# Optimization experiments

Measured on AMD Instinct MI355X. Metric: run time of the kernel, lower is better.

The kernel has to match this reference:

```python
import jax, jax.numpy as jnp
import numpy as np

N_NODES = 10000
N_EDGES = 320000
HID = 256
EDGE_D = 2
NORM_FACTOR = 100.0
NORM_CONST = 1.0


def setup_inputs() -> dict:
    key = jax.random.key(0)
    ks = jax.random.split(key, 32)
    s = 0.02
    d = {
        'h': jax.random.normal(ks[0], (N_NODES, HID), jnp.float32),
        'x': jax.random.normal(ks[1], (N_NODES, 3), jnp.float32),
        'edge_index': jax.random.randint(ks[2], (2, N_EDGES), 0, N_NODES, jnp.int32),
        'edge_attr': jax.random.uniform(ks[3], (N_EDGES, EDGE_D), jnp.float32),
    }
    in_e = 2 * HID + EDGE_D  # 514
    ki = 4
    for li in range(2):
        p = f'gcl{li}_'
        d[p + 'ew1'] = jax.random.normal(ks[ki], (in_e, HID), jnp.float32) * s; ki += 1
        d[p + 'eb1'] = jnp.zeros((HID,), jnp.float32)
        d[p + 'ew2'] = jax.random.normal(ks[ki], (HID, HID), jnp.float32) * s; ki += 1
        d[p + 'eb2'] = jnp.zeros((HID,), jnp.float32)
        d[p + 'nw1'] = jax.random.normal(ks[ki], (2 * HID, HID), jnp.float32) * s; ki += 1
        d[p + 'nb1'] = jnp.zeros((HID,), jnp.float32)
        d[p + 'nw2'] = jax.random.normal(ks[ki], (HID, HID), jnp.float32) * s; ki += 1
        d[p + 'nb2'] = jnp.zeros((HID,), jnp.float32)
        d[p + 'aw'] = jax.random.normal(ks[ki], (HID, 1), jnp.float32) * s; ki += 1
        d[p + 'ab'] = jnp.zeros((1,), jnp.float32)
    d['cw1'] = jax.random.normal(ks[ki], (in_e, HID), jnp.float32) * s; ki += 1
    d['cb1'] = jnp.zeros((HID,), jnp.float32)
    d['cw2'] = jax.random.normal(ks[ki], (HID, HID), jnp.float32) * s; ki += 1
    d['cb2'] = jnp.zeros((HID,), jnp.float32)
    # xavier_uniform with gain=0.001 -> very small final layer
    d['cw3'] = jax.random.normal(ks[ki], (HID, 1), jnp.float32) * 0.001
    return d


def _gcl(h, row, col, edge_attr, ew1, eb1, ew2, eb2, nw1, nb1, nw2, nb2, aw, ab, n_nodes):
    inp = jnp.concatenate([h[row], h[col], edge_attr], axis=1)  # [E, 2H+2]
    mij = jax.nn.silu(jax.nn.silu(inp @ ew1 + eb1) @ ew2 + eb2)  # [E, H]
    att = jax.nn.sigmoid(mij @ aw + ab)                          # [E, 1]
    ef = mij * att
    agg = jax.ops.segment_sum(ef, row, num_segments=n_nodes) / NORM_FACTOR
    nin = jnp.concatenate([h, agg], axis=1)                      # [N, 2H]
    return h + (jax.nn.silu(nin @ nw1 + nb1) @ nw2 + nb2)


def reference(h, x, edge_index, edge_attr,
              gcl0_ew1, gcl0_eb1, gcl0_ew2, gcl0_eb2, gcl0_nw1, gcl0_nb1, gcl0_nw2, gcl0_nb2, gcl0_aw, gcl0_ab,
              gcl1_ew1, gcl1_eb1, gcl1_ew2, gcl1_eb2, gcl1_nw1, gcl1_nb1, gcl1_nw2, gcl1_nb2, gcl1_aw, gcl1_ab,
              cw1, cb1, cw2, cb2, cw3):
    n_nodes = h.shape[0]
    row, col = edge_index[0], edge_index[1]
    # coord2diff (norm_constant = 1)
    diff = x[row] - x[col]                                  # [E, 3]
    radial = jnp.sum(diff * diff, axis=1, keepdims=True)    # [E, 1]
    norm = jnp.sqrt(radial + 1e-8)
    coord_diff = diff / (norm + NORM_CONST)
    # two GCL layers (reflection_equiv=True -> no cross product)
    h = _gcl(h, row, col, edge_attr, gcl0_ew1, gcl0_eb1, gcl0_ew2, gcl0_eb2,
             gcl0_nw1, gcl0_nb1, gcl0_nw2, gcl0_nb2, gcl0_aw, gcl0_ab, n_nodes)
    h = _gcl(h, row, col, edge_attr, gcl1_ew1, gcl1_eb1, gcl1_ew2, gcl1_eb2,
             gcl1_nw1, gcl1_nb1, gcl1_nw2, gcl1_nb2, gcl1_aw, gcl1_ab, n_nodes)
    # equivariant coordinate update (tanh=False)
    inp = jnp.concatenate([h[row], h[col], edge_attr], axis=1)
    phi = jax.nn.silu(jax.nn.silu(inp @ cw1 + cb1) @ cw2 + cb2) @ cw3  # [E, 1]
    trans = coord_diff * phi                                            # [E, 3]
    agg = jax.ops.segment_sum(trans, row, num_segments=n_nodes) / NORM_FACTOR
    x = x + agg
    return h, x
```

## Files before the change

### kernel.cpp

```cpp
#include <hip/hip_runtime.h>
#include <hip/hip_fp16.h>
#include <stdint.h>

#define NN   10000
#define NE   320000
#define HID  256
#define MB   64
#define NEB  (NE/MB)
#define VST  264

#define DG_PLAIN 0
#define DG_SPLIT 1
#define DG_2A    2

typedef __attribute__((ext_vector_type(8))) short short8;
typedef __attribute__((ext_vector_type(4))) float f32x4;

struct CvtPtrs { const float* p[15]; };

__device__ __forceinline__ float silu_f(float v){ return v / (1.f + __expf(-v)); }
__device__ __forceinline__ float sigm_f(float v){ return 1.f / (1.f + __expf(-v)); }
__device__ __forceinline__ __half2 silu2(__half2 x){
    __half2 e = h2exp2(__hmul2(x, __float2half2_rn(-1.442695041f)));
    __half2 d = __hadd2(e, __float2half2_rn(1.0f));
    return __hmul2(x, h2rcp(d));
}

__global__ __launch_bounds__(256) void k_count(const int* __restrict__ row, int* __restrict__ cnt){
    int e = blockIdx.x * 256 + threadIdx.x;
    if (e < NE) atomicAdd(&cnt[row[e]], 1);
}

__global__ __launch_bounds__(256) void k_scan(const int* __restrict__ cnt, int* __restrict__ rs, int* __restrict__ cur){
    __shared__ int sums[256];
    const int PER = 40;
    int t = threadIdx.x;
    int base = t * PER;
    int s = 0;
    for (int i = 0; i < PER; i++){
        int idx = base + i;
        s += (idx < NN) ? cnt[idx] : 0;
    }
    sums[t] = s;
    __syncthreads();
    for (int off = 1; off < 256; off <<= 1){
        int v = (t >= off) ? sums[t - off] : 0;
        __syncthreads();
        sums[t] += v;
        __syncthreads();
    }
    int run = (t == 0) ? 0 : sums[t - 1];
    for (int i = 0; i < PER; i++){
        int idx = base + i;
        if (idx < NN){
            int c = cnt[idx];
            rs[idx] = run;
            cur[idx] = run;
            run += c;
        }
    }
    if (t == 255) rs[NN] = sums[255];
}

__global__ __launch_bounds__(256) void k_fill(const int* __restrict__ row, int* __restrict__ cur, int* __restrict__ perm){
    int e = blockIdx.x * 256 + threadIdx.x;
    if (e < NE){
        int p = atomicAdd(&cur[row[e]], 1);
        perm[p] = e;
    }
}

__global__ __launch_bounds__(256) void k_cvtw(CvtPtrs pp, __half* __restrict__ dst){
    int i = blockIdx.x * 256 + threadIdx.x;
    const float* src = pp.p[i >> 16];
    int t = i & 65535;
    int j = t & 7, lane = (t >> 3) & 63, kk = (t >> 9) & 7, nt = t >> 12;
    int k = kk * 32 + (lane >> 4) * 8 + j;
    int n = nt * 16 + (lane & 15);
    dst[i] = __float2half_rn(src[k * HID + n]);
}

__global__ __launch_bounds__(256) void k_cvt16(const float* __restrict__ src, __half* __restrict__ dst){
    int i = (blockIdx.x * 256 + threadIdx.x) * 8;
    float4 f0 = *(const float4*)&src[i];
    float4 f1 = *(const float4*)&src[i + 4];
    uint4 o; __half2* op = (__half2*)&o;
    op[0] = __float22half2_rn(make_float2(f0.x, f0.y));
    op[1] = __float22half2_rn(make_float2(f0.z, f0.w));
    op[2] = __float22half2_rn(make_float2(f1.x, f1.y));
    op[3] = __float22half2_rn(make_float2(f1.z, f1.w));
    *(uint4*)&dst[i] = o;
}

__global__ __launch_bounds__(256, 4) void k_dgemm(
        const __half* __restrict__ A1, const float* __restrict__ A2f,
        const __half* __restrict__ wpool, int wAidx, int wBidx,
        const float* __restrict__ bias, const float* __restrict__ R,
        float* __restrict__ out32, __half* __restrict__ out16,
        __half* __restrict__ outB16, int mode, int act){
    __shared__ __half alds[64 * VST];
    int tid = threadIdx.x;
    int lid = tid & 63, w = tid >> 6;
    int quad = lid >> 4, l15 = lid & 15;
    int rb = blockIdx.x * 64;
    int by = blockIdx.y;

    float bv[2]; int cg0[2];
    #pragma unroll
    for (int n = 0; n < 2; n++){
        int cg = by * 128 + w * 32 + n * 16 + l15;
        cg0[n] = cg;
        bv[n] = (bias && cg < 256) ? bias[cg] : 0.f;
    }
    f32x4 acc[4][2];
    #pragma unroll
    for (int m = 0; m < 4; m++)
        #pragma unroll
        for (int n = 0; n < 2; n++){ f32x4 z = {bv[n], bv[n], bv[n], bv[n]}; acc[m][n] = z; }

    int npass = (mode == DG_2A) ? 2 : 1;
    int sr = tid >> 5, c0 = (tid & 31) * 8;
    for (int pass = 0; pass < npass; pass++){
        if (pass) __syncthreads();
        int widx, byl = by;
        if (mode == DG_SPLIT){ if (by >= 2){ widx = wBidx; byl = by - 2; } else widx = wAidx; }
        else widx = pass ? wBidx : wAidx;
        const short8* bbase = (const short8*)(wpool + (size_t)widx * 65536);

        if (pass == 0){
            #pragma unroll
            for (int it = 0; it < 8; it++){
                int r = it * 8 + sr;
                int rr = rb + r; if (rr > NN - 1) rr = NN - 1;
                *(uint4*)&alds[r * VST + c0] = *(const uint4*)&A1[(size_t)rr * HID + c0];
            }
        } else {
            #pragma unroll
            for (int it = 0; it < 8; it++){
                int r = it * 8 + sr;
                int rr = rb + r; if (rr > NN - 1) rr = NN - 1;
                float4 f0 = *(const float4*)&A2f[(size_t)rr * HID + c0];
                float4 f1 = *(const float4*)&A2f[(size_t)rr * HID + c0 + 4];
                uint4 o; __half2* op = (__half2*)&o;
                op[0] = __float22half2_rn(make_float2(f0.x, f0.y));
                op[1] = __float22half2_rn(make_float2(f0.z, f0.w));
                op[2] = __float22half2_rn(make_float2(f1.x, f1.y));
                op[3] = __float22half2_rn(make_float2(f1.z, f1.w));
                *(uint4*)&alds[r * VST + c0] = o;
            }
        }
        __syncthreads();
        #pragma unroll
        for (int kk = 0; kk < 8; kk++){
            short8 bf[2];
            #pragma unroll
            for (int n = 0; n < 2; n++)
                bf[n] = bbase[((byl * 8 + w * 2 + n) * 8 + kk) * 64 + lid];
            #pragma unroll
            for (int m = 0; m < 4; m++){
                const short8 af = *(const short8*)&alds[(m * 16 + l15) * VST + kk * 32 + quad * 8];
                #pragma unroll
                for (int n = 0; n < 2; n++)
                    acc[m][n] = __builtin_amdgcn_mfma_f32_16x16x32_f16(af, bf[n], acc[m][n], 0, 0, 0);
            }
        }
    }
    #pragma unroll
    for (int n = 0; n < 2; n++){
        int cg = cg0[n];
        #pragma unroll
        for (int m = 0; m < 4; m++){
            #pragma unroll
            for (int r = 0; r < 4; r++){
                int rg = rb + m * 16 + quad * 4 + r;
                if (rg < NN){
                    float v = acc[m][n][r];
                    if (act) v = silu_f(v);
                    if (R) v += R[(size_t)rg * HID + cg];
                    if (mode == DG_SPLIT){
                        if (cg < 256) out16[(size_t)rg * HID + cg] = __float2half_rn(v);
                        else          outB16[(size_t)rg * HID + cg - 256] = __float2half_rn(v);
                    } else {
                        if (out32) out32[(size_t)rg * HID + cg] = v;
                        if (out16) out16[(size_t)rg * HID + cg] = __float2half_rn(v);
                    }
                }
            }
        }
    }
}

__global__ __launch_bounds__(256, 4) void k_edge_mfma(
        const __half* __restrict__ HrowB, const __half* __restrict__ HcolB,
        const int* __restrict__ row, const int* __restrict__ col,
        const float* __restrict__ ea, const int* __restrict__ perm,
        const __half* __restrict__ w2f,
        const float* __restrict__ w512, const float* __restrict__ w513,
        const float* __restrict__ eb2, const float* __restrict__ aw, const float* __restrict__ ab,
        float* __restrict__ agg){
    __shared__ __half vlds[MB * VST];
    __shared__ float attp[4][MB];
    __shared__ float attf[MB];
    __shared__ int   nrows[MB];
    __shared__ int   cids[MB];
    __shared__ float ea0s[MB], ea1s[MB];

    int tid = threadIdx.x;
    int e0  = blockIdx.x * MB;
    if (tid < MB){
        int eid = perm[e0 + tid];
        nrows[tid] = row[eid];
        cids[tid]  = col[eid];
        ea0s[tid]  = ea[eid * 2 + 0];
        ea1s[tid]  = ea[eid * 2 + 1];
    }
    __syncthreads();
    {
        int sr = tid >> 5;
        int c0 = (tid & 31) * 8;
        float4 wa = *(const float4*)&w512[c0];
        float4 wb = *(const float4*)&w512[c0 + 4];
        float4 ua = *(const float4*)&w513[c0];
        float4 ub = *(const float4*)&w513[c0 + 4];
        __half2 w5h[4] = {__float22half2_rn(make_float2(wa.x, wa.y)), __float22half2_rn(make_float2(wa.z, wa.w)),
                          __float22half2_rn(make_float2(wb.x, wb.y)), __float22half2_rn(make_float2(wb.z, wb.w))};
        __half2 w6h[4] = {__float22half2_rn(make_float2(ua.x, ua.y)), __float22half2_rn(make_float2(ua.z, ua.w)),
                          __float22half2_rn(make_float2(ub.x, ub.y)), __float22half2_rn(make_float2(ub.z, ub.w))};
        #pragma unroll
        for (int it = 0; it < 8; it++){
            int r = it * 8 + sr;
            int nid = nrows[r], cid = cids[r];
            __half2 e0h = __float2half2_rn(ea0s[r]);
            __half2 e1h = __float2half2_rn(ea1s[r]);
            uint4 hr4 = *(const uint4*)&HrowB[(size_t)nid * HID + c0];
            uint4 hc4 = *(const uint4*)&HcolB[(size_t)cid * HID + c0];
            const __half2* hrp = (const __half2*)&hr4;
            const __half2* hcp = (const __half2*)&hc4;
            uint4 o; __half2* op = (__half2*)&o;
            #pragma unroll
            for (int q = 0; q < 4; q++){
                __half2 t = __hadd2(hrp[q], hcp[q]);
                t = __hfma2(e0h, w5h[q], t);
                t = __hfma2(e1h, w6h[q], t);
                op[q] = silu2(t);
            }
            *(uint4*)&vlds[r * VST + c0] = o;
        }
    }
    __syncthreads();

    int lid = tid & 63, w = tid >> 6;
    int quad = lid >> 4, l15 = lid & 15;

    float b2v[4], awv[4];
    #pragma unroll
    for (int n = 0; n < 4; n++){
        int cg = w * 64 + n * 16 + l15;
        b2v[n] = eb2[cg]; awv[n] = aw[cg];
    }
    f32x4 acc[4][4];
    #pragma unroll
    for (int m = 0; m < 4; m++)
        #pragma unroll
        for (int n = 0; n < 4; n++){ f32x4 z = {b2v[n], b2v[n], b2v[n], b2v[n]}; acc[m][n] = z; }

    const short8* bbase = (const short8*)w2f;
    #pragma unroll
    for (int kk = 0; kk < 8; kk++){
        short8 bf[4];
        #pragma unroll
        for (int n = 0; n < 4; n++)
            bf[n] = bbase[((w * 4 + n) * 8 + kk) * 64 + lid];
        #pragma unroll
        for (int m = 0; m < 4; m++){
            const short8 af = *(const short8*)&vlds[(m * 16 + l15) * VST + kk * 32 + quad * 8];
            #pragma unroll
            for (int n = 0; n < 4; n++)
                acc[m][n] = __builtin_amdgcn_mfma_f32_16x16x32_f16(af, bf[n], acc[m][n], 0, 0, 0);
        }
    }

    #pragma unroll
    for (int m = 0; m < 4; m++){
        float p[4] = {0.f, 0.f, 0.f, 0.f};
        #pragma unroll
        for (int n = 0; n < 4; n++){
            #pragma unroll
            for (int r = 0; r < 4; r++){
                float mij = silu_f(acc[m][n][r]);
                acc[m][n][r] = mij;
                p[r] += mij * awv[n];
            }
        }
        #pragma unroll
        for (int r = 0; r < 4; r++){
            p[r] += __shfl_xor(p[r], 1);
            p[r] += __shfl_xor(p[r], 2);
            p[r] += __shfl_xor(p[r], 4);
            p[r] += __shfl_xor(p[r], 8);
        }
        if (l15 == 0){
            #pragma unroll
            for (int r = 0; r < 4; r++)
                attp[w][m * 16 + quad * 4 + r] = p[r];
        }
    }
    __syncthreads();
    if (tid < MB){
        float a0 = attp[0][tid] + attp[1][tid] + attp[2][tid] + attp[3][tid] + ab[0];
        attf[tid] = 0.01f * sigm_f(a0);
    }
    __syncthreads();

    for (int m = 0; m < 4; m++){
        int mb = m * 16;
        float av[4]; int nv[4];
        #pragma unroll
        for (int r = 0; r < 4; r++){
            av[r] = attf[mb + quad * 4 + r];
            nv[r] = nrows[mb + quad * 4 + r];
        }
        int rA = nrows[mb], rB = nrows[mb + 15];
        if (rA == rB){
            #pragma unroll
            for (int n = 0; n < 4; n++){
                float s = acc[m][n][0] * av[0] + acc[m][n][1] * av[1]
                        + acc[m][n][2] * av[2] + acc[m][n][3] * av[3];
                s += __shfl_xor(s, 16);
                s += __shfl_xor(s, 32);
                if (lid < 16)
                    atomicAdd(&agg[(size_t)rA * HID + w * 64 + n * 16 + lid], s);
            }
        } else {
            float ef[4][4];
            #pragma unroll
            for (int n = 0; n < 4; n++)
                #pragma unroll
                for (int r = 0; r < 4; r++)
                    ef[n][r] = acc[m][n][r] * av[r];
            int myn = nrows[mb + l15];
            int t16 = 0;
            while (t16 < 16){
                int tgt = nrows[mb + t16];
                unsigned long long bal = __ballot((lid < 16) && (lid > t16) && (myn != tgt));
                int nxt = bal ? (__ffsll((unsigned long long)bal) - 1) : 16;
                #pragma unroll
                for (int n = 0; n < 4; n++){
                    float s = 0.f;
                    #pragma unroll
                    for (int r = 0; r < 4; r++)
                        s += (nv[r] == tgt) ? ef[n][r] : 0.f;
                    s += __shfl_xor(s, 16);
                    s += __shfl_xor(s, 32);
                    if (lid < 16)
                        atomicAdd(&agg[(size_t)tgt * HID + w * 64 + n * 16 + lid], s);
                }
                t16 = nxt;
            }
        }
    }
}

__global__ __launch_bounds__(256, 4) void k_coord_mfma(
        const __half* __restrict__ CrowB, const __half* __restrict__ CcolB,
        const int* __restrict__ row, const int* __restrict__ col,
        const float* __restrict__ ea, const int* __restrict__ perm,
        const __half* __restrict__ w2f,
        const float* __restrict__ w512, const float* __restrict__ w513,
        const float* __restrict__ cb2, const float* __restrict__ cw3,
        float* __restrict__ phi){
    __shared__ __half vlds[MB * VST];
    __shared__ float pp[4][MB];
    __shared__ int   nrows[MB];
    __shared__ int   cids[MB];
    __shared__ float ea0s[MB], ea1s[MB];

    int tid = threadIdx.x;
    int e0  = blockIdx.x * MB;
    if (tid < MB){
        int eid = perm[e0 + tid];
        nrows[tid] = row[eid];
        cids[tid]  = col[eid];
        ea0s[tid]  = ea[eid * 2 + 0];
        ea1s[tid]  = ea[eid * 2 + 1];
    }
    __syncthreads();
    {
        int sr = tid >> 5;
        int c0 = (tid & 31) * 8;
        float4 wa = *(const float4*)&w512[c0];
        float4 wb = *(const float4*)&w512[c0 + 4];
        float4 ua = *(const float4*)&w513[c0];
        float4 ub = *(const float4*)&w513[c0 + 4];
        __half2 w5h[4] = {__float22half2_rn(make_float2(wa.x, wa.y)), __float22half2_rn(make_float2(wa.z, wa.w)),
                          __float22half2_rn(make_float2(wb.x, wb.y)), __float22half2_rn(make_float2(wb.z, wb.w))};
        __half2 w6h[4] = {__float22half2_rn(make_float2(ua.x, ua.y)), __float22half2_rn(make_float2(ua.z, ua.w)),
                          __float22half2_rn(make_float2(ub.x, ub.y)), __float22half2_rn(make_float2(ub.z, ub.w))};
        #pragma unroll
        for (int it = 0; it < 8; it++){
            int r = it * 8 + sr;
            int nid = nrows[r], cid = cids[r];
            __half2 e0h = __float2half2_rn(ea0s[r]);
            __half2 e1h = __float2half2_rn(ea1s[r]);
            uint4 hr4 = *(const uint4*)&CrowB[(size_t)nid * HID + c0];
            uint4 hc4 = *(const uint4*)&CcolB[(size_t)cid * HID + c0];
            const __half2* hrp = (const __half2*)&hr4;
            const __half2* hcp = (const __half2*)&hc4;
            uint4 o; __half2* op = (__half2*)&o;
            #pragma unroll
            for (int q = 0; q < 4; q++){
                __half2 t = __hadd2(hrp[q], hcp[q]);
                t = __hfma2(e0h, w5h[q], t);
                t = __hfma2(e1h, w6h[q], t);
                op[q] = silu2(t);
            }
            *(uint4*)&vlds[r * VST + c0] = o;
        }
    }
    __syncthreads();

    int lid = tid & 63, w = tid >> 6;
    int quad = lid >> 4, l15 = lid & 15;

    float b2v[4], w3v[4];
    #pragma unroll
    for (int n = 0; n < 4; n++){
        int cg = w * 64 + n * 16 + l15;
        b2v[n] = cb2[cg]; w3v[n] = cw3[cg];
    }
    f32x4 acc[4][4];
    #pragma unroll
    for (int m = 0; m < 4; m++)
        #pragma unroll
        for (int n = 0; n < 4; n++){ f32x4 z = {b2v[n], b2v[n], b2v[n], b2v[n]}; acc[m][n] = z; }

    const short8* bbase = (const short8*)w2f;
    #pragma unroll
    for (int kk = 0; kk < 8; kk++){
        short8 bf[4];
        #pragma unroll
        for (int n = 0; n < 4; n++)
            bf[n] = bbase[((w * 4 + n) * 8 + kk) * 64 + lid];
        #pragma unroll
        for (int m = 0; m < 4; m++){
            const short8 af = *(const short8*)&vlds[(m * 16 + l15) * VST + kk * 32 + quad * 8];
            #pragma unroll
            for (int n = 0; n < 4; n++)
                acc[m][n] = __builtin_amdgcn_mfma_f32_16x16x32_f16(af, bf[n], acc[m][n], 0, 0, 0);
        }
    }

    #pragma unroll
    for (int m = 0; m < 4; m++){
        float p[4] = {0.f, 0.f, 0.f, 0.f};
        #pragma unroll
        for (int n = 0; n < 4; n++)
            #pragma unroll
            for (int r = 0; r < 4; r++)
                p[r] += silu_f(acc[m][n][r]) * w3v[n];
        #pragma unroll
        for (int r = 0; r < 4; r++){
            p[r] += __shfl_xor(p[r], 1);
            p[r] += __shfl_xor(p[r], 2);
            p[r] += __shfl_xor(p[r], 4);
            p[r] += __shfl_xor(p[r], 8);
        }
        if (l15 == 0){
            #pragma unroll
            for (int r = 0; r < 4; r++)
                pp[w][m * 16 + quad * 4 + r] = p[r];
        }
    }
    __syncthreads();
    if (tid < MB)
        phi[e0 + tid] = pp[0][tid] + pp[1][tid] + pp[2][tid] + pp[3][tid];
}

__global__ __launch_bounds__(64) void k_xupd(const float* __restrict__ x, const float* __restrict__ phi,
                                             const int* __restrict__ col, const int* __restrict__ perm,
                                             const int* __restrict__ rs, float* __restrict__ xout){
    int n = blockIdx.x, lid = threadIdx.x;
    int s = rs[n], e = rs[n + 1];
    float x0 = x[n * 3 + 0], x1 = x[n * 3 + 1], x2 = x[n * 3 + 2];
    float tx = 0.f, ty = 0.f, tz = 0.f;
    for (int i = s + lid; i < e; i += 64){
        int eid = perm[i];
        int c = col[eid];
        float d0 = x0 - x[c * 3 + 0];
        float d1 = x1 - x[c * 3 + 1];
        float d2 = x2 - x[c * 3 + 2];
        float r2 = d0 * d0 + d1 * d1 + d2 * d2;
        float f  = phi[i] / (sqrtf(r2 + 1e-8f) + 1.f);
        tx += d0 * f; ty += d1 * f; tz += d2 * f;
    }
    for (int o = 32; o; o >>= 1){
        tx += __shfl_down(tx, o);
        ty += __shfl_down(ty, o);
        tz += __shfl_down(tz, o);
    }
    if (lid == 0){
        xout[n * 3 + 0] = x0 + 0.01f * tx;
        xout[n * 3 + 1] = x1 + 0.01f * ty;
        xout[n * 3 + 2] = x2 + 0.01f * tz;
    }
}

extern "C" void kernel_launch(void* const* d_in, const int* in_sizes, int n_in,
                              void* d_out, int out_size, void* d_ws, size_t ws_size,
                              hipStream_t stream){
    const float* h  = (const float*)d_in[0];
    const float* x  = (const float*)d_in[1];
    const int*   ei = (const int*)d_in[2];
    const float* ea = (const float*)d_in[3];
    const int* rowp = ei;
    const int* colp = ei + NE;

    const float* ew1[2] = {(const float*)d_in[4],  (const float*)d_in[14]};
    const float* eb1[2] = {(const float*)d_in[5],  (const float*)d_in[15]};
    const float* ew2[2] = {(const float*)d_in[6],  (const float*)d_in[16]};
    const float* eb2[2] = {(const float*)d_in[7],  (const float*)d_in[17]};
    const float* nw1[2] = {(const float*)d_in[8],  (const float*)d_in[18]};
    const float* nb1[2] = {(const float*)d_in[9],  (const float*)d_in[19]};
    const float* nw2[2] = {(const float*)d_in[10], (const float*)d_in[20]};
    const float* nb2[2] = {(const float*)d_in[11], (const float*)d_in[21]};
    const float* aw[2]  = {(const float*)d_in[12], (const float*)d_in[22]};
    const float* ab[2]  = {(const float*)d_in[13], (const float*)d_in[23]};
    const float* cw1 = (const float*)d_in[24];
    const float* cb1 = (const float*)d_in[25];
    const float* cw2 = (const float*)d_in[26];
    const float* cb2 = (const float*)d_in[27];
    const float* cw3 = (const float*)d_in[28];

    char* w = (char*)d_ws;
    auto alloc = [&](size_t bytes){ void* p = (void*)w; w += (bytes + 255) & ~((size_t)255); return p; };
    int* rs    = (int*)alloc((NN + 1) * sizeof(int));
    int* cur   = (int*)alloc(NN * sizeof(int));
    int* perm  = (int*)alloc(NE * sizeof(int));
    __half* HrowB = (__half*)alloc((size_t)NN * HID * sizeof(__half));
    __half* HcolB = (__half*)alloc((size_t)NN * HID * sizeof(__half));
    float*  aggb  = (float*)alloc((size_t)NN * HID * sizeof(float));
    __half* wfrag = (__half*)alloc((size_t)15 * HID * HID * sizeof(__half));
    float*  phi   = (float*)alloc((size_t)NE * sizeof(float));
    __half* h16   = (__half*)alloc((size_t)NN * HID * sizeof(__half));
    __half* Tb16  = HrowB;

    float* hout = (float*)d_out;
    float* xout = hout + (size_t)NN * HID;

    hipMemsetAsync(cur, 0, NN * sizeof(int), stream);
    k_count<<<(NE + 255) / 256, 256, 0, stream>>>(rowp, cur);
    k_scan<<<1, 256, 0, stream>>>(cur, rs, cur);
    k_fill<<<(NE + 255) / 256, 256, 0, stream>>>(rowp, cur, perm);

    CvtPtrs cp;
    for (int l = 0; l < 2; l++){
        cp.p[l * 5 + 0] = ew1[l];
        cp.p[l * 5 + 1] = ew1[l] + 256 * HID;
        cp.p[l * 5 + 2] = nw1[l];
        cp.p[l * 5 + 3] = nw1[l] + 256 * HID;
        cp.p[l * 5 + 4] = nw2[l];
    }
    cp.p[10] = cw1;
    cp.p[11] = cw1 + 256 * HID;
    cp.p[12] = ew2[0];
    cp.p[13] = ew2[1];
    cp.p[14] = cw2;
    k_cvtw<<<15 * 256, 256, 0, stream>>>(cp, wfrag);
    k_cvt16<<<1250, 256, 0, stream>>>(h, h16);

    dim3 g2(157, 2), g4(157, 4);
    const float* hres = h;
    for (int l = 0; l < 2; l++){
        k_dgemm<<<g4, 256, 0, stream>>>(h16, nullptr, wfrag, l * 5 + 0, l * 5 + 1,
                                        eb1[l], nullptr, nullptr, HrowB, HcolB, DG_SPLIT, 0);
        hipMemsetAsync(aggb, 0, (size_t)NN * HID * sizeof(float), stream);
        k_edge_mfma<<<NEB, 256, 0, stream>>>(HrowB, HcolB, rowp, colp, ea, perm,
                                             wfrag + (size_t)(12 + l) * HID * HID,
                                             ew1[l] + 512 * HID, ew1[l] + 513 * HID,
                                             eb2[l], aw[l], ab[l], aggb);
        k_dgemm<<<g2, 256, 0, stream>>>(h16, aggb, wfrag, l * 5 + 2, l * 5 + 3,
                                        nb1[l], nullptr, nullptr, Tb16, nullptr, DG_2A, 1);
        k_dgemm<<<g2, 256, 0, stream>>>(Tb16, nullptr, wfrag, l * 5 + 4, 0,
                                        nb2[l], hres, hout, h16, nullptr, DG_PLAIN, 0);
        hres = hout;
    }
    k_dgemm<<<g4, 256, 0, stream>>>(h16, nullptr, wfrag, 10, 11,
                                    cb1, nullptr, nullptr, HrowB, HcolB, DG_SPLIT, 0);
    k_coord_mfma<<<NEB, 256, 0, stream>>>(HrowB, HcolB, rowp, colp, ea, perm,
                                          wfrag + (size_t)14 * HID * HID,
                                          cw1 + 512 * HID, cw1 + 513 * HID,
                                          cb2, cw3, phi);
    k_xupd<<<NN, 64, 0, stream>>>(x, phi, colp, perm, rs, xout);
}
```

Before: 609.9 us.

## XOR-swizzle LDS tiles and move edge-MLP epilogue to packed half math

Removes the padded LDS row stride (264) in the dense GEMM and edge kernels and uses an XOR swizzle on 16-byte column groups instead. This avoids bank conflicts with less LDS, which could allow more resident blocks. The edge and coordinate epilogues now do SiLU, the attention/phi dot product and the shuffle reductions in packed __half2 arithmetic rather than fp32. That halves the ALU and shuffle work but adds fp16 rounding to the attention logits, phi and the messages.

```diff
diff --git a/kernel.cpp b/kernel.cpp
--- a/kernel.cpp
+++ b/kernel.cpp
@@ -7,7 +7,6 @@
 #define HID  256
 #define MB   64
 #define NEB  (NE/MB)
-#define VST  264
 
 #define DG_PLAIN 0
 #define DG_SPLIT 1
@@ -24,6 +23,12 @@
     __half2 e = h2exp2(__hmul2(x, __float2half2_rn(-1.442695041f)));
     __half2 d = __hadd2(e, __float2half2_rn(1.0f));
     return __hmul2(x, h2rcp(d));
+}
+__device__ __forceinline__ __half2 h2shfl_xor_add(__half2 v, int m){
+    int pi = *(int*)&v;
+    pi = __shfl_xor(pi, m, 64);
+    __half2 q = *(__half2*)&pi;
+    return __hadd2(v, q);
 }
 
 __global__ __launch_bounds__(256) void k_count(const int* __restrict__ row, int* __restrict__ cnt){
@@ -98,12 +103,13 @@
         const float* __restrict__ bias, const float* __restrict__ R,
         float* __restrict__ out32, __half* __restrict__ out16,
         __half* __restrict__ outB16, int mode, int act){
-    __shared__ __half alds[64 * VST];
+    __shared__ __half alds[64 * 256];
     int tid = threadIdx.x;
     int lid = tid & 63, w = tid >> 6;
     int quad = lid >> 4, l15 = lid & 15;
     int rb = blockIdx.x * 64;
     int by = blockIdx.y;
+    int xorv = l15 & 7;
 
     float bv[2]; int cg0[2];
     #pragma unroll
@@ -119,7 +125,9 @@
         for (int n = 0; n < 2; n++){ f32x4 z = {bv[n], bv[n], bv[n], bv[n]}; acc[m][n] = z; }
 
     int npass = (mode == DG_2A) ? 2 : 1;
-    int sr = tid >> 5, c0 = (tid & 31) * 8;
+    int sr = tid >> 5;
+    int c0 = (tid & 31) * 8;
+    int pc = (((tid & 31) ^ sr) * 8);
     for (int pass = 0; pass < npass; pass++){
         if (pass) __syncthreads();
         int widx, byl = by;
@@ -132,7 +140,7 @@
             for (int it = 0; it < 8; it++){
                 int r = it * 8 + sr;
                 int rr = rb + r; if (rr > NN - 1) rr = NN - 1;
-                *(uint4*)&alds[r * VST + c0] = *(const uint4*)&A1[(size_t)rr * HID + c0];
+                *(uint4*)&alds[r * 256 + pc] = *(const uint4*)&A1[(size_t)rr * HID + c0];
             }
         } else {
             #pragma unroll
@@ -146,7 +154,7 @@
                 op[1] = __float22half2_rn(make_float2(f0.z, f0.w));
                 op[2] = __float22half2_rn(make_float2(f1.x, f1.y));
                 op[3] = __float22half2_rn(make_float2(f1.z, f1.w));
-                *(uint4*)&alds[r * VST + c0] = o;
+                *(uint4*)&alds[r * 256 + pc] = o;
             }
         }
         __syncthreads();
@@ -158,7 +166,7 @@
                 bf[n] = bbase[((byl * 8 + w * 2 + n) * 8 + kk) * 64 + lid];
             #pragma unroll
             for (int m = 0; m < 4; m++){
-                const short8 af = *(const short8*)&alds[(m * 16 + l15) * VST + kk * 32 + quad * 8];
+                const short8 af = *(const short8*)&alds[(m * 16 + l15) * 256 + (((kk * 4 + quad) ^ xorv) * 8)];
                 #pragma unroll
                 for (int n = 0; n < 2; n++)
                     acc[m][n] = __builtin_amdgcn_mfma_f32_16x16x32_f16(af, bf[n], acc[m][n], 0, 0, 0);
@@ -198,8 +206,8 @@
         const float* __restrict__ w512, const float* __restrict__ w513,
         const float* __restrict__ eb2, const float* __restrict__ aw, const float* __restrict__ ab,
         float* __restrict__ agg){
-    __shared__ __half vlds[MB * VST];
-    __shared__ float attp[4][MB];
+    __shared__ __half vlds[MB * 256];
+    __shared__ unsigned int attp2[4][MB / 2];
     __shared__ float attf[MB];
     __shared__ int   nrows[MB];
     __shared__ int   cids[MB];
@@ -207,6 +215,7 @@
 
     int tid = threadIdx.x;
     int e0  = blockIdx.x * MB;
+    float ab0 = ab[0];
     if (tid < MB){
         int eid = perm[e0 + tid];
         nrows[tid] = row[eid];
@@ -218,6 +227,7 @@
     {
         int sr = tid >> 5;
         int c0 = (tid & 31) * 8;
+        int pc = ((tid & 31) ^ sr) * 8;
         float4 wa = *(const float4*)&w512[c0];
         float4 wb = *(const float4*)&w512[c0 + 4];
         float4 ua = *(const float4*)&w513[c0];
@@ -244,19 +254,21 @@
                 t = __hfma2(e1h, w6h[q], t);
                 op[q] = silu2(t);
             }
-            *(uint4*)&vlds[r * VST + c0] = o;
+            *(uint4*)&vlds[r * 256 + pc] = o;
         }
     }
     __syncthreads();
 
     int lid = tid & 63, w = tid >> 6;
     int quad = lid >> 4, l15 = lid & 15;
-
-    float b2v[4], awv[4];
+    int xorv = l15 & 7;
+
+    float b2v[4]; __half2 aw2[4];
     #pragma unroll
     for (int n = 0; n < 4; n++){
         int cg = w * 64 + n * 16 + l15;
-        b2v[n] = eb2[cg]; awv[n] = aw[cg];
+        b2v[n] = eb2[cg];
+        aw2[n] = __float2half2_rn(aw[cg]);
     }
     f32x4 acc[4][4];
     #pragma unroll
@@ -273,71 +285,73 @@
             bf[n] = bbase[((w * 4 + n) * 8 + kk) * 64 + lid];
         #pragma unroll
         for (int m = 0; m < 4; m++){
-            const short8 af = *(const short8*)&vlds[(m * 16 + l15) * VST + kk * 32 + quad * 8];
+            const short8 af = *(const short8*)&vlds[(m * 16 + l15) * 256 + (((kk * 4 + quad) ^ xorv) * 8)];
             #pragma unroll
             for (int n = 0; n < 4; n++)
                 acc[m][n] = __builtin_amdgcn_mfma_f32_16x16x32_f16(af, bf[n], acc[m][n], 0, 0, 0);
         }
     }
 
+    __half2 mijp[4][4][2];
     #pragma unroll
     for (int m = 0; m < 4; m++){
-        float p[4] = {0.f, 0.f, 0.f, 0.f};
+        __half2 p2a = __float2half2_rn(0.f), p2b = p2a;
         #pragma unroll
         for (int n = 0; n < 4; n++){
-            #pragma unroll
-            for (int r = 0; r < 4; r++){
-                float mij = silu_f(acc[m][n][r]);
-                acc[m][n][r] = mij;
-                p[r] += mij * awv[n];
-            }
-        }
-        #pragma unroll
-        for (int r = 0; r < 4; r++){
-            p[r] += __shfl_xor(p[r], 1);
-            p[r] += __shfl_xor(p[r], 2);
-            p[r] += __shfl_xor(p[r], 4);
-            p[r] += __shfl_xor(p[r], 8);
-        }
+            __half2 ha = silu2(__float22half2_rn(make_float2(acc[m][n][0], acc[m][n][1])));
+            __half2 hb = silu2(__float22half2_rn(make_float2(acc[m][n][2], acc[m][n][3])));
+            mijp[m][n][0] = ha; mijp[m][n][1] = hb;
+            p2a = __hfma2(ha, aw2[n], p2a);
+            p2b = __hfma2(hb, aw2[n], p2b);
+        }
+        p2a = h2shfl_xor_add(p2a, 1); p2a = h2shfl_xor_add(p2a, 2);
+        p2a = h2shfl_xor_add(p2a, 4); p2a = h2shfl_xor_add(p2a, 8);
+        p2b = h2shfl_xor_add(p2b, 1); p2b = h2shfl_xor_add(p2b, 2);
+        p2b = h2shfl_xor_add(p2b, 4); p2b = h2shfl_xor_add(p2b, 8);
         if (l15 == 0){
-            #pragma unroll
-            for (int r = 0; r < 4; r++)
-                attp[w][m * 16 + quad * 4 + r] = p[r];
+            attp2[w][m * 8 + quad * 2 + 0] = *(unsigned int*)&p2a;
+            attp2[w][m * 8 + quad * 2 + 1] = *(unsigned int*)&p2b;
         }
     }
     __syncthreads();
     if (tid < MB){
-        float a0 = attp[0][tid] + attp[1][tid] + attp[2][tid] + attp[3][tid] + ab[0];
+        int pr = tid >> 1;
+        unsigned int u0 = attp2[0][pr], u1 = attp2[1][pr], u2 = attp2[2][pr], u3 = attp2[3][pr];
+        __half2 h0 = *(__half2*)&u0, h1 = *(__half2*)&u1, h2 = *(__half2*)&u2, h3 = *(__half2*)&u3;
+        float lo = __low2float(h0) + __low2float(h1) + __low2float(h2) + __low2float(h3);
+        float hi = __high2float(h0) + __high2float(h1) + __high2float(h2) + __high2float(h3);
+        float a0 = ((tid & 1) ? hi : lo) + ab0;
         attf[tid] = 0.01f * sigm_f(a0);
     }
     __syncthreads();
 
     for (int m = 0; m < 4; m++){
         int mb = m * 16;
-        float av[4]; int nv[4];
-        #pragma unroll
-        for (int r = 0; r < 4; r++){
-            av[r] = attf[mb + quad * 4 + r];
-            nv[r] = nrows[mb + quad * 4 + r];
-        }
+        __half2 at2a = __float22half2_rn(make_float2(attf[mb + quad * 4 + 0], attf[mb + quad * 4 + 1]));
+        __half2 at2b = __float22half2_rn(make_float2(attf[mb + quad * 4 + 2], attf[mb + quad * 4 + 3]));
         int rA = nrows[mb], rB = nrows[mb + 15];
         if (rA == rB){
             #pragma unroll
             for (int n = 0; n < 4; n++){
-                float s = acc[m][n][0] * av[0] + acc[m][n][1] * av[1]
-                        + acc[m][n][2] * av[2] + acc[m][n][3] * av[3];
+                __half2 s2 = __hmul2(mijp[m][n][0], at2a);
+                s2 = __hfma2(mijp[m][n][1], at2b, s2);
+                float s = __low2float(s2) + __high2float(s2);
                 s += __shfl_xor(s, 16);
                 s += __shfl_xor(s, 32);
                 if (lid < 16)
                     atomicAdd(&agg[(size_t)rA * HID + w * 64 + n * 16 + lid], s);
             }
         } else {
-            float ef[4][4];
-            #pragma unroll
-            for (int n = 0; n < 4; n++)
-                #pragma unroll
-                for (int r = 0; r < 4; r++)
-                    ef[n][r] = acc[m][n][r] * av[r];
+            float ef[4][4]; int nv[4];
+            #pragma unroll
+            for (int r = 0; r < 4; r++) nv[r] = nrows[mb + quad * 4 + r];
+            #pragma unroll
+            for (int n = 0; n < 4; n++){
+                __half2 ea2 = __hmul2(mijp[m][n][0], at2a);
+                __half2 eb2h = __hmul2(mijp[m][n][1], at2b);
+                ef[n][0] = __low2float(ea2);  ef[n][1] = __high2float(ea2);
+                ef[n][2] = __low2float(eb2h); ef[n][3] = __high2float(eb2h);
+            }
             int myn = nrows[mb + l15];
             int t16 = 0;
             while (t16 < 16){
@@ -369,8 +383,8 @@
         const float* __restrict__ w512, const float* __restrict__ w513,
         const float* __restrict__ cb2, const float* __restrict__ cw3,
         float* __restrict__ phi){
-    __shared__ __half vlds[MB * VST];
-    __shared__ float pp[4][MB];
+    __shared__ __half vlds[MB * 256];
+    __shared__ unsigned int pp2[4][MB / 2];
     __shared__ int   nrows[MB];
     __shared__ int   cids[MB];
     __shared__ float ea0s[MB], ea1s[MB];
@@ -388,6 +402,7 @@
     {
         int sr = tid >> 5;
         int c0 = (tid & 31) * 8;
+        int pc = ((tid & 31) ^ sr) * 8;
         float4 wa = *(const float4*)&w512[c0];
         float4 wb = *(const float4*)&w512[c0 + 4];
         float4 ua = *(const float4*)&w513[c0];
@@ -414,19 +429,21 @@
                 t = __hfma2(e1h, w6h[q], t);
                 op[q] = silu2(t);
             }
-            *(uint4*)&vlds[r * VST + c0] = o;
+            *(uint4*)&vlds[r * 256 + pc] = o;
         }
     }
     __syncthreads();
 
     int lid = tid & 63, w = tid >> 6;
     int quad = lid >> 4, l15 = lid & 15;
-
-    float b2v[4], w3v[4];
+    int xorv = l15 & 7;
+
+    float b2v[4]; __half2 w32[4];
     #pragma unroll
     for (int n = 0; n < 4; n++){
         int cg = w * 64 + n * 16 + l15;
-        b2v[n] = cb2[cg]; w3v[n] = cw3[cg];
+        b2v[n] = cb2[cg];
+        w32[n] = __float2half2_rn(cw3[cg]);
     }
     f32x4 acc[4][4];
     #pragma unroll
@@ -443,7 +460,7 @@
             bf[n] = bbase[((w * 4 + n) * 8 + kk) * 64 + lid];
         #pragma unroll
         for (int m = 0; m < 4; m++){
-            const short8 af = *(const short8*)&vlds[(m * 16 + l15) * VST + kk * 32 + quad * 8];
+            const short8 af = *(const short8*)&vlds[(m * 16 + l15) * 256 + (((kk * 4 + quad) ^ xorv) * 8)];
             #pragma unroll
             for (int n = 0; n < 4; n++)
                 acc[m][n] = __builtin_amdgcn_mfma_f32_16x16x32_f16(af, bf[n], acc[m][n], 0, 0, 0);
@@ -452,28 +469,32 @@
 
     #pragma unroll
     for (int m = 0; m < 4; m++){
-        float p[4] = {0.f, 0.f, 0.f, 0.f};
-        #pragma unroll
-        for (int n = 0; n < 4; n++)
-            #pragma unroll
-            for (int r = 0; r < 4; r++)
-                p[r] += silu_f(acc[m][n][r]) * w3v[n];
-        #pragma unroll
-        for (int r = 0; r < 4; r++){
-            p[r] += __shfl_xor(p[r], 1);
-            p[r] += __shfl_xor(p[r], 2);
-            p[r] += __shfl_xor(p[r], 4);
-            p[r] += __shfl_xor(p[r], 8);
-        }
+        __half2 p2a = __float2half2_rn(0.f), p2b = p2a;
+        #pragma unroll
+        for (int n = 0; n < 4; n++){
+            __half2 ha = silu2(__float22half2_rn(make_float2(acc[m][n][0], acc[m][n][1])));
+            __half2 hb = silu2(__float22half2_rn(make_float2(acc[m][n][2], acc[m][n][3])));
+            p2a = __hfma2(ha, w32[n], p2a);
+            p2b = __hfma2(hb, w32[n], p2b);
+        }
+        p2a = h2shfl_xor_add(p2a, 1); p2a = h2shfl_xor_add(p2a, 2);
+        p2a = h2shfl_xor_add(p2a, 4); p2a = h2shfl_xor_add(p2a, 8);
+        p2b = h2shfl_xor_add(p2b, 1); p2b = h2shfl_xor_add(p2b, 2);
+        p2b = h2shfl_xor_add(p2b, 4); p2b = h2shfl_xor_add(p2b, 8);
         if (l15 == 0){
-            #pragma unroll
-            for (int r = 0; r < 4; r++)
-                pp[w][m * 16 + quad * 4 + r] = p[r];
-        }
-    }
-    __syncthreads();
-    if (tid < MB)
-        phi[e0 + tid] = pp[0][tid] + pp[1][tid] + pp[2][tid] + pp[3][tid];
+            pp2[w][m * 8 + quad * 2 + 0] = *(unsigned int*)&p2a;
+            pp2[w][m * 8 + quad * 2 + 1] = *(unsigned int*)&p2b;
+        }
+    }
+    __syncthreads();
+    if (tid < MB){
+        int pr = tid >> 1;
+        unsigned int u0 = pp2[0][pr], u1 = pp2[1][pr], u2 = pp2[2][pr], u3 = pp2[3][pr];
+        __half2 h0 = *(__half2*)&u0, h1 = *(__half2*)&u1, h2 = *(__half2*)&u2, h3 = *(__half2*)&u3;
+        float lo = __low2float(h0) + __low2float(h1) + __low2float(h2) + __low2float(h3);
+        float hi = __high2float(h0) + __high2float(h1) + __high2float(h2) + __high2float(h3);
+        phi[e0 + tid] = (tid & 1) ? hi : lo;
+    }
 }
 
 __global__ __launch_bounds__(64) void k_xupd(const float* __restrict__ x, const float* __restrict__ phi,
```

Result: faster. 561.1 us (-8.0%).
